# Optimization experiments

Measured on AMD Instinct MI355X. Metric: run time of the kernel, lower is better.

The kernel has to match this reference:

```python
import jax, jax.numpy as jnp
import numpy as np

N, E, G = 100000, 1600000, 256
D, H, O, DEPTH = 128, 128, 128, 3
BN_EPS = 1e-5
LN_EPS = 1e-5


def setup_inputs() -> dict:
    key = jax.random.key(0)
    ks = jax.random.split(key, 16)
    x = jax.random.normal(ks[0], (N, D), dtype=jnp.float32)
    edge_index = jax.random.randint(ks[1], (2, E), 0, N, dtype=jnp.int64)
    batch = jnp.sort(jax.random.randint(ks[2], (N,), 0, G, dtype=jnp.int64))
    s1 = 1.0 / np.sqrt(D)
    s2 = 1.0 / np.sqrt(H)
    return {
        "x": x,
        "edge_index": edge_index,
        "batch": batch,
        "W1s": jax.random.normal(ks[3], (DEPTH, D, H), dtype=jnp.float32) * s1,
        "b1s": jax.random.normal(ks[4], (DEPTH, H), dtype=jnp.float32) * 0.01,
        "bn_g": jnp.ones((DEPTH, H), dtype=jnp.float32),
        "bn_b": jnp.zeros((DEPTH, H), dtype=jnp.float32),
        "bn_m": jax.random.normal(ks[5], (DEPTH, H), dtype=jnp.float32) * 0.1,
        "bn_v": jax.random.uniform(ks[6], (DEPTH, H), dtype=jnp.float32, minval=0.5, maxval=1.5),
        "W2s": jax.random.normal(ks[7], (DEPTH, H, H), dtype=jnp.float32) * s2,
        "b2s": jax.random.normal(ks[8], (DEPTH, H), dtype=jnp.float32) * 0.01,
        "Wp": jax.random.normal(ks[9], (H, O), dtype=jnp.float32) * s2,
        "bp": jax.random.normal(ks[10], (O,), dtype=jnp.float32) * 0.01,
        "ln_g": jnp.ones((O,), dtype=jnp.float32),
        "ln_b": jnp.zeros((O,), dtype=jnp.float32),
    }


def reference(x, edge_index, batch, W1s, b1s, bn_g, bn_b, bn_m, bn_v, W2s, b2s, Wp, bp, ln_g, ln_b):
    src, dst = edge_index[0], edge_index[1]
    h = x
    for l in range(DEPTH):
        # GIN aggregation (eps=0): (1+eps)*h_i + sum_{j->i} h_j
        agg = jax.ops.segment_sum(h[src], dst, num_segments=N)  # [N, H]
        z = h + agg
        # MLP: Linear -> BatchNorm(eval) -> ReLU -> Linear
        z = z @ W1s[l] + b1s[l]
        z = (z - bn_m[l]) * jax.lax.rsqrt(bn_v[l] + BN_EPS) * bn_g[l] + bn_b[l]
        z = jax.nn.relu(z)
        z = z @ W2s[l] + b2s[l]
        # post-conv ReLU (dropout = identity in eval)
        h = jax.nn.relu(z)
    # global mean pool over graphs
    counts = jax.ops.segment_sum(jnp.ones((N,), h.dtype), batch, num_segments=G)
    hg = jax.ops.segment_sum(h, batch, num_segments=G) / jnp.maximum(counts, 1.0)[:, None]
    # proj: Linear + LayerNorm
    p = hg @ Wp + bp
    mu = jnp.mean(p, axis=-1, keepdims=True)
    var = jnp.var(p, axis=-1, keepdims=True)
    return (p - mu) * jax.lax.rsqrt(var + LN_EPS) * ln_g + ln_b
```

## Files before the change

kernel.cpp:

```cpp
#include <hip/hip_runtime.h>
#include <hip/hip_bf16.h>


#define GDEPTH 3
#define CAP 64

typedef __bf16 bf16x8 __attribute__((ext_vector_type(8)));
typedef float  f32x4  __attribute__((ext_vector_type(4)));
typedef __hip_bfloat16  bf16;
typedef __hip_bfloat162 bf162;

#define CSR_CH 2048
#define NSLICE 8
#define NSLICE_LOG 3

__global__ void k_setup(const float* __restrict__ W1s, const float* __restrict__ W2s,
                        const float* __restrict__ b1s, const float* __restrict__ bng,
                        const float* __restrict__ bnb, const float* __restrict__ bnm,
                        const float* __restrict__ bnv,
                        bf16* __restrict__ Wp1, bf16* __restrict__ Wp2,
                        float* __restrict__ sArr, float* __restrict__ tArr,
                        const float4* __restrict__ x4, bf162* __restrict__ h,
                        const int* __restrict__ batch, int* __restrict__ gp,
                        const int* __restrict__ ei, int* __restrict__ fill,
                        int* __restrict__ col,
                        int N, int E, int G, int BCONV, int BGB, int BCSR) {
    int bid = blockIdx.x;
    int tid = threadIdx.x;
    if (bid % 3 == 0 && bid / 3 < BCSR) {
        int sb = bid / 3;
        int s = sb & (NSLICE - 1);
        int chunk = sb >> NSLICE_LOG;
        int lo = (int)((long long)s * N / NSLICE);
        int hi = (int)((long long)(s + 1) * N / NSLICE);
        int baseq = chunk * (CSR_CH / 4);
        const int4* d4p = (const int4*)(ei + E);
        const int4* s4p = (const int4*)ei;
        #pragma unroll
        for (int i = 0; i < CSR_CH / 1024; ++i) {
            int q = baseq + i * 256 + tid;
            int e0 = q * 4;
            if (e0 + 3 < E) {
                int4 d4 = d4p[q];
                if ((d4.x >= lo && d4.x < hi) || (d4.y >= lo && d4.y < hi) ||
                    (d4.z >= lo && d4.z < hi) || (d4.w >= lo && d4.w < hi)) {
                    int4 s4 = s4p[q];
                    if (d4.x >= lo && d4.x < hi) { int p = atomicAdd(&fill[d4.x], 1); if (p < CAP) col[(size_t)d4.x * CAP + p] = s4.x; }
                    if (d4.y >= lo && d4.y < hi) { int p = atomicAdd(&fill[d4.y], 1); if (p < CAP) col[(size_t)d4.y * CAP + p] = s4.y; }
                    if (d4.z >= lo && d4.z < hi) { int p = atomicAdd(&fill[d4.z], 1); if (p < CAP) col[(size_t)d4.z * CAP + p] = s4.z; }
                    if (d4.w >= lo && d4.w < hi) { int p = atomicAdd(&fill[d4.w], 1); if (p < CAP) col[(size_t)d4.w * CAP + p] = s4.w; }
                }
            } else if (e0 < E) {
                for (int e = e0; e < E; ++e) {
                    int d = ei[E + e];
                    if (d >= lo && d < hi) {
                        int p = atomicAdd(&fill[d], 1);
                        if (p < CAP) col[(size_t)d * CAP + p] = ei[e];
                    }
                }
            }
        }
        return;
    }
    {
        int nsc = (bid + 2) / 3;
        if (nsc > BCSR) nsc = BCSR;
        bid -= nsc;
    }
    if (bid < 384) {
        int idx = bid * 256 + tid;
        int l   = idx / 32768;
        int rem = idx - l * 32768;
        int w   = rem >> 14;
        int p   = rem & 16383;
        int j = p & 7, n = (p >> 3) & 127, tq = p >> 10;
        int quad = tq & 3, kk = tq >> 2;
        int k = kk * 32 + quad * 8 + j;
        const float* W = w ? W2s : W1s;
        bf16* Wp = w ? Wp2 : Wp1;
        Wp[l * 16384 + p] = __float2bfloat16(W[l * 16384 + k * 128 + n]);
        if (idx < GDEPTH * 128) {
            int ll = idx >> 7, c = idx & 127;
            float inv = rsqrtf(bnv[ll * 128 + c] + 1e-5f);
            float s = inv * bng[ll * 128 + c];
            sArr[idx] = s;
            tArr[idx] = (b1s[ll * 128 + c] - bnm[ll * 128 + c]) * s + bnb[ll * 128 + c];
        }
        return;
    }
    bid -= 384;
    if (bid < BCONV) {
        int i = bid * 256 + tid;
        int n4 = N * 32;
        if (i < n4) {
            float4 v = x4[i];
            bf162 a, b;
            a.x = __float2bfloat16(v.x); a.y = __float2bfloat16(v.y);
            b.x = __float2bfloat16(v.z); b.y = __float2bfloat16(v.w);
            h[2 * i] = a; h[2 * i + 1] = b;
        }
        return;
    }
    bid -= BCONV;
    if (bid < BGB) {
        int i = bid * 256 + tid;
        if (i < N) {
            int b = batch[i];
            if (i == 0) {
                for (int g = 0; g <= b; ++g) gp[g] = 0;
            } else {
                int pb = batch[i - 1];
                if (pb != b) for (int g = pb + 1; g <= b; ++g) gp[g] = i;
            }
            if (i == N - 1) {
                for (int g = b + 1; g <= G; ++g) gp[g] = N;
            }
        }
        return;
    }
}

__global__ __launch_bounds__(256) void k_layer(const bf16* __restrict__ h,
                                               const int* __restrict__ deg,
                                               const int* __restrict__ col,
                                               const bf16* __restrict__ Bp1,
                                               const bf16* __restrict__ Bp2,
                                               const float* __restrict__ sv,
                                               const float* __restrict__ tv,
                                               const float* __restrict__ b2,
                                               bf16* __restrict__ Out, int M) {
    __shared__ __align__(16) bf16 As[32 * 136];
    const int tid = threadIdx.x;
    const int m0 = blockIdx.x * 32;
    const int grp = tid >> 4, c = tid & 15;
    const bf16x8* h8 = (const bf16x8*)h;

    #pragma unroll
    for (int it = 0; it < 2; ++it) {
        int row = grp * 2 + it;
        int node = m0 + row;
        float acc[8];
        if (node < M) {
            bf16x8 self = h8[(size_t)node * 16 + c];
            #pragma unroll
            for (int k = 0; k < 8; ++k) acc[k] = (float)self[k];
            int d = deg[node]; if (d > CAP) d = CAP;
            const int* cb = col + (size_t)node * CAP;
            int e = 0;
            for (; e + 3 < d; e += 4) {
                int j0 = cb[e], j1 = cb[e + 1], j2 = cb[e + 2], j3 = cb[e + 3];
                bf16x8 v0 = h8[(size_t)j0 * 16 + c];
                bf16x8 v1 = h8[(size_t)j1 * 16 + c];
                bf16x8 v2 = h8[(size_t)j2 * 16 + c];
                bf16x8 v3 = h8[(size_t)j3 * 16 + c];
                #pragma unroll
                for (int k = 0; k < 8; ++k)
                    acc[k] += ((float)v0[k] + (float)v1[k]) + ((float)v2[k] + (float)v3[k]);
            }
            for (; e < d; ++e) {
                bf16x8 v = h8[(size_t)cb[e] * 16 + c];
                #pragma unroll
                for (int k = 0; k < 8; ++k) acc[k] += (float)v[k];
            }
        } else {
            #pragma unroll
            for (int k = 0; k < 8; ++k) acc[k] = 0.f;
        }
        bf16x8 r;
        #pragma unroll
        for (int k = 0; k < 8; ++k) {
            __hip_bfloat16 t = __float2bfloat16(acc[k]);
            r[k] = *(__bf16*)&t;
        }
        *(bf16x8*)(As + row * 136 + c * 8) = r;
    }
    __syncthreads();

    const int lane = tid & 63;
    const int wid = tid >> 6;
    const int wm = wid & 1, wn = wid >> 1;
    const int l15 = lane & 15, quad = lane >> 4;

    f32x4 acc[4];
    #pragma unroll
    for (int j = 0; j < 4; ++j) acc[j] = (f32x4){0.f, 0.f, 0.f, 0.f};
    #pragma unroll
    for (int kk = 0; kk < 4; ++kk) {
        bf16x8 a, b[4];
        #pragma unroll
        for (int tn = 0; tn < 4; ++tn)
            b[tn] = *(const bf16x8*)(Bp1 + ((kk * 4 + quad) * 128 + wn * 64 + tn * 16 + l15) * 8);
        a = *(const bf16x8*)(As + (wm * 16 + l15) * 136 + kk * 32 + quad * 8);
        #pragma unroll
        for (int tn = 0; tn < 4; ++tn)
            acc[tn] = __builtin_amdgcn_mfma_f32_16x16x32_bf16(a, b[tn], acc[tn], 0, 0, 0);
    }
    __syncthreads();
    #pragma unroll
    for (int tn = 0; tn < 4; ++tn) {
        int gc = wn * 64 + tn * 16 + l15;
        float scale = sv[gc], shift = tv[gc];
        #pragma unroll
        for (int r = 0; r < 4; ++r) {
            float v = fmaxf(acc[tn][r] * scale + shift, 0.f);
            int row = wm * 16 + quad * 4 + r;
            __hip_bfloat16 t = __float2bfloat16(v);
            As[row * 136 + gc] = *(bf16*)&t;
        }
    }
    __syncthreads();
    #pragma unroll
    for (int j = 0; j < 4; ++j) acc[j] = (f32x4){0.f, 0.f, 0.f, 0.f};
    #pragma unroll
    for (int kk = 0; kk < 4; ++kk) {
        bf16x8 a, b[4];
        #pragma unroll
        for (int tn = 0; tn < 4; ++tn)
            b[tn] = *(const bf16x8*)(Bp2 + ((kk * 4 + quad) * 128 + wn * 64 + tn * 16 + l15) * 8);
        a = *(const bf16x8*)(As + (wm * 16 + l15) * 136 + kk * 32 + quad * 8);
        #pragma unroll
        for (int tn = 0; tn < 4; ++tn)
            acc[tn] = __builtin_amdgcn_mfma_f32_16x16x32_bf16(a, b[tn], acc[tn], 0, 0, 0);
    }
    #pragma unroll
    for (int tn = 0; tn < 4; ++tn) {
        int gc = wn * 64 + tn * 16 + l15;
        float shift = b2[gc];
        #pragma unroll
        for (int r = 0; r < 4; ++r) {
            int gr = m0 + wm * 16 + quad * 4 + r;
            if (gr < M) {
                float v = fmaxf(acc[tn][r] + shift, 0.f);
                Out[(size_t)gr * 128 + gc] = __float2bfloat16(v);
            }
        }
    }
}

#define PCH 128
__global__ void k_pool(const bf16* __restrict__ h, const int* __restrict__ batch,
                       float* __restrict__ hga, int N) {
    int base = blockIdx.x * PCH;
    if (base >= N) return;
    int t = threadIdx.x;
    int end = base + PCH; if (end > N) end = N;
    int gcur = batch[base];
    float acc = 0.f;
    for (int i = base; i < end; ++i) {
        int g = batch[i];
        if (g != gcur) {
            atomicAdd(&hga[gcur * 128 + t], acc);
            acc = 0.f; gcur = g;
        }
        acc += __bfloat162float(h[(size_t)i * 128 + t]);
    }
    atomicAdd(&hga[gcur * 128 + t], acc);
}

__global__ void k_proj_ln(const float* __restrict__ hga, const int* __restrict__ gp,
                          const float* __restrict__ Wp,
                          const float* __restrict__ bp, const float* __restrict__ lng,
                          const float* __restrict__ lnb, float* __restrict__ out) {
    __shared__ float row[128];
    __shared__ float red[128];
    int g = blockIdx.x, t = threadIdx.x;
    int cntn = gp[g + 1] - gp[g];
    float inv = 1.0f / (float)(cntn < 1 ? 1 : cntn);
    row[t] = hga[g * 128 + t] * inv;
    __syncthreads();
    float p = bp[t];
    #pragma unroll 8
    for (int k = 0; k < 128; ++k) p += row[k] * Wp[k * 128 + t];
    red[t] = p; __syncthreads();
    for (int o = 64; o > 0; o >>= 1) { if (t < o) red[t] += red[t + o]; __syncthreads(); }
    float mu = red[0] * (1.0f / 128.0f);
    __syncthreads();
    float d = p - mu;
    red[t] = d * d; __syncthreads();
    for (int o = 64; o > 0; o >>= 1) { if (t < o) red[t] += red[t + o]; __syncthreads(); }
    float var = red[0] * (1.0f / 128.0f);
    out[g * 128 + t] = d * rsqrtf(var + 1e-5f) * lng[t] + lnb[t];
}

extern "C" void kernel_launch(void* const* d_in, const int* in_sizes, int n_in,
                              void* d_out, int out_size, void* d_ws, size_t ws_size,
                              hipStream_t stream) {
    const float* x   = (const float*)d_in[0];
    const int*   ei  = (const int*)d_in[1];
    const int*   bat = (const int*)d_in[2];
    const float* W1s = (const float*)d_in[3];
    const float* b1s = (const float*)d_in[4];
    const float* bng = (const float*)d_in[5];
    const float* bnb = (const float*)d_in[6];
    const float* bnm = (const float*)d_in[7];
    const float* bnv = (const float*)d_in[8];
    const float* W2s = (const float*)d_in[9];
    const float* b2s = (const float*)d_in[10];
    const float* Wp  = (const float*)d_in[11];
    const float* bp  = (const float*)d_in[12];
    const float* lng = (const float*)d_in[13];
    const float* lnb = (const float*)d_in[14];
    const int E = in_sizes[1] / 2;
    const int N = in_sizes[2];
    const int G = out_size / 128;

    char* w = (char*)d_ws;
    size_t off = 0;
    auto alloc = [&](size_t b) { char* p = w + off; off += (b + 255) & ~(size_t)255; return p; };
    bf16* buf_a = (bf16*)alloc((size_t)N * 128 * 2);
    bf16* buf_b = (bf16*)alloc((size_t)N * 128 * 2);
    int* col   = (int*)alloc(((size_t)N * CAP + 256) * 4);
    int* fill  = (int*)alloc((size_t)N * 4);
    float* hga = (float*)alloc((size_t)G * 128 * 4);
    int* gp    = (int*)alloc(2048);
    bf16* Wp1  = (bf16*)alloc((size_t)GDEPTH * 16384 * 2);
    bf16* Wp2  = (bf16*)alloc((size_t)GDEPTH * 16384 * 2);
    float* sA  = (float*)alloc((size_t)GDEPTH * 128 * 4);
    float* tA  = (float*)alloc((size_t)GDEPTH * 128 * 4);

    size_t zlen = (size_t)((char*)hga + (size_t)G * 128 * 4 - (char*)fill);
    hipMemsetAsync(fill, 0, zlen, stream);

    const int BCONV = (N * 32 + 255) / 256;
    const int BGB   = (N + 255) / 256;
    const int BCSR  = ((E + CSR_CH - 1) / CSR_CH) * NSLICE;
    k_setup<<<384 + BCONV + BGB + BCSR, 256, 0, stream>>>(
        W1s, W2s, b1s, bng, bnb, bnm, bnv, Wp1, Wp2, sA, tA,
        (const float4*)x, (bf162*)buf_a, bat, gp, ei, fill, col, N, E, G, BCONV, BGB, BCSR);

    const bf16* hcur = buf_a;
    bf16* hnext = buf_b;
    for (int l = 0; l < GDEPTH; ++l) {
        k_layer<<<(N + 31) / 32, 256, 0, stream>>>(hcur, fill, col,
                                                   Wp1 + (size_t)l * 16384,
                                                   Wp2 + (size_t)l * 16384,
                                                   sA + l * 128, tA + l * 128,
                                                   b2s + l * 128, hnext, N);
        bf16* tmp = hnext; hnext = (bf16*)hcur; hcur = tmp;
    }
    k_pool<<<(N + PCH - 1) / PCH, 128, 0, stream>>>(hcur, bat, hga, N);
    k_proj_ln<<<G, 128, 0, stream>>>(hga, gp, Wp, bp, lng, lnb, (float*)d_out);
}
```

Before: 472.3 us.

## Fuse layers, pooling and projection into one persistent cooperative kernel

Replaces the three per-layer launches plus the pool and projection kernels with a single cooperative persistent kernel. Blocks loop over row tiles and use grid-wide syncs between layers and phases. The aim is to remove launch overhead and the tail gaps between kernels. The trade-offs are grid.sync costs, a grid capped by occupancy (up to 2048 blocks with a launch bound of 4 per SM), and a pooling phase that uses fewer parallel chunks per block.

```diff
diff --git a/kernel.cpp b/kernel.cpp
--- a/kernel.cpp
+++ b/kernel.cpp
@@ -1,9 +1,13 @@
 #include <hip/hip_runtime.h>
 #include <hip/hip_bf16.h>
+#include <hip/hip_cooperative_groups.h>
+
+namespace cg = cooperative_groups;
 
 
 #define GDEPTH 3
 #define CAP 64
+#define PCH 128
 
 typedef __bf16 bf16x8 __attribute__((ext_vector_type(8)));
 typedef float  f32x4  __attribute__((ext_vector_type(4)));
@@ -120,166 +124,192 @@
     }
 }
 
-__global__ __launch_bounds__(256) void k_layer(const bf16* __restrict__ h,
-                                               const int* __restrict__ deg,
-                                               const int* __restrict__ col,
-                                               const bf16* __restrict__ Bp1,
-                                               const bf16* __restrict__ Bp2,
-                                               const float* __restrict__ sv,
-                                               const float* __restrict__ tv,
-                                               const float* __restrict__ b2,
-                                               bf16* __restrict__ Out, int M) {
-    __shared__ __align__(16) bf16 As[32 * 136];
+__global__ __launch_bounds__(256, 4) void k_mega(
+        bf16* __restrict__ bufA, bf16* __restrict__ bufB,
+        const int* __restrict__ deg, const int* __restrict__ col,
+        const bf16* __restrict__ Wp1, const bf16* __restrict__ Wp2,
+        const float* __restrict__ sAr, const float* __restrict__ tAr,
+        const float* __restrict__ b2s,
+        const int* __restrict__ batch, const int* __restrict__ gp,
+        float* __restrict__ hga,
+        const float* __restrict__ Wpj, const float* __restrict__ bpj,
+        const float* __restrict__ lng, const float* __restrict__ lnb,
+        float* __restrict__ outp,
+        int N, int G, int NT, int NB) {
+    cg::grid_group gg = cg::this_grid();
+    __shared__ __align__(16) char smem[32 * 136 * 2];
+    bf16* As = (bf16*)smem;
     const int tid = threadIdx.x;
-    const int m0 = blockIdx.x * 32;
-    const int grp = tid >> 4, c = tid & 15;
-    const bf16x8* h8 = (const bf16x8*)h;
-
-    #pragma unroll
-    for (int it = 0; it < 2; ++it) {
-        int row = grp * 2 + it;
-        int node = m0 + row;
-        float acc[8];
-        if (node < M) {
-            bf16x8 self = h8[(size_t)node * 16 + c];
-            #pragma unroll
-            for (int k = 0; k < 8; ++k) acc[k] = (float)self[k];
-            int d = deg[node]; if (d > CAP) d = CAP;
-            const int* cb = col + (size_t)node * CAP;
-            int e = 0;
-            for (; e + 3 < d; e += 4) {
-                int j0 = cb[e], j1 = cb[e + 1], j2 = cb[e + 2], j3 = cb[e + 3];
-                bf16x8 v0 = h8[(size_t)j0 * 16 + c];
-                bf16x8 v1 = h8[(size_t)j1 * 16 + c];
-                bf16x8 v2 = h8[(size_t)j2 * 16 + c];
-                bf16x8 v3 = h8[(size_t)j3 * 16 + c];
-                #pragma unroll
-                for (int k = 0; k < 8; ++k)
-                    acc[k] += ((float)v0[k] + (float)v1[k]) + ((float)v2[k] + (float)v3[k]);
-            }
-            for (; e < d; ++e) {
-                bf16x8 v = h8[(size_t)cb[e] * 16 + c];
-                #pragma unroll
-                for (int k = 0; k < 8; ++k) acc[k] += (float)v[k];
-            }
-        } else {
-            #pragma unroll
-            for (int k = 0; k < 8; ++k) acc[k] = 0.f;
-        }
-        bf16x8 r;
-        #pragma unroll
-        for (int k = 0; k < 8; ++k) {
-            __hip_bfloat16 t = __float2bfloat16(acc[k]);
-            r[k] = *(__bf16*)&t;
-        }
-        *(bf16x8*)(As + row * 136 + c * 8) = r;
-    }
-    __syncthreads();
-
-    const int lane = tid & 63;
-    const int wid = tid >> 6;
-    const int wm = wid & 1, wn = wid >> 1;
-    const int l15 = lane & 15, quad = lane >> 4;
-
-    f32x4 acc[4];
-    #pragma unroll
-    for (int j = 0; j < 4; ++j) acc[j] = (f32x4){0.f, 0.f, 0.f, 0.f};
-    #pragma unroll
-    for (int kk = 0; kk < 4; ++kk) {
-        bf16x8 a, b[4];
-        #pragma unroll
-        for (int tn = 0; tn < 4; ++tn)
-            b[tn] = *(const bf16x8*)(Bp1 + ((kk * 4 + quad) * 128 + wn * 64 + tn * 16 + l15) * 8);
-        a = *(const bf16x8*)(As + (wm * 16 + l15) * 136 + kk * 32 + quad * 8);
-        #pragma unroll
-        for (int tn = 0; tn < 4; ++tn)
-            acc[tn] = __builtin_amdgcn_mfma_f32_16x16x32_bf16(a, b[tn], acc[tn], 0, 0, 0);
-    }
-    __syncthreads();
-    #pragma unroll
-    for (int tn = 0; tn < 4; ++tn) {
-        int gc = wn * 64 + tn * 16 + l15;
-        float scale = sv[gc], shift = tv[gc];
-        #pragma unroll
-        for (int r = 0; r < 4; ++r) {
-            float v = fmaxf(acc[tn][r] * scale + shift, 0.f);
-            int row = wm * 16 + quad * 4 + r;
-            __hip_bfloat16 t = __float2bfloat16(v);
-            As[row * 136 + gc] = *(bf16*)&t;
-        }
-    }
-    __syncthreads();
-    #pragma unroll
-    for (int j = 0; j < 4; ++j) acc[j] = (f32x4){0.f, 0.f, 0.f, 0.f};
-    #pragma unroll
-    for (int kk = 0; kk < 4; ++kk) {
-        bf16x8 a, b[4];
-        #pragma unroll
-        for (int tn = 0; tn < 4; ++tn)
-            b[tn] = *(const bf16x8*)(Bp2 + ((kk * 4 + quad) * 128 + wn * 64 + tn * 16 + l15) * 8);
-        a = *(const bf16x8*)(As + (wm * 16 + l15) * 136 + kk * 32 + quad * 8);
-        #pragma unroll
-        for (int tn = 0; tn < 4; ++tn)
-            acc[tn] = __builtin_amdgcn_mfma_f32_16x16x32_bf16(a, b[tn], acc[tn], 0, 0, 0);
-    }
-    #pragma unroll
-    for (int tn = 0; tn < 4; ++tn) {
-        int gc = wn * 64 + tn * 16 + l15;
-        float shift = b2[gc];
-        #pragma unroll
-        for (int r = 0; r < 4; ++r) {
-            int gr = m0 + wm * 16 + quad * 4 + r;
-            if (gr < M) {
-                float v = fmaxf(acc[tn][r] + shift, 0.f);
-                Out[(size_t)gr * 128 + gc] = __float2bfloat16(v);
-            }
-        }
-    }
-}
-
-#define PCH 128
-__global__ void k_pool(const bf16* __restrict__ h, const int* __restrict__ batch,
-                       float* __restrict__ hga, int N) {
-    int base = blockIdx.x * PCH;
-    if (base >= N) return;
-    int t = threadIdx.x;
-    int end = base + PCH; if (end > N) end = N;
-    int gcur = batch[base];
-    float acc = 0.f;
-    for (int i = base; i < end; ++i) {
-        int g = batch[i];
-        if (g != gcur) {
+
+    for (int l = 0; l < GDEPTH; ++l) {
+        const bf16* h = (l & 1) ? bufB : bufA;
+        bf16* Out = (l & 1) ? bufA : bufB;
+        const bf16* Bp1 = Wp1 + (size_t)l * 16384;
+        const bf16* Bp2 = Wp2 + (size_t)l * 16384;
+        const float* sv = sAr + l * 128;
+        const float* tv = tAr + l * 128;
+        const float* b2 = b2s + l * 128;
+        const bf16x8* h8 = (const bf16x8*)h;
+
+        for (int tile = blockIdx.x; tile < NT; tile += NB) {
+            const int m0 = tile * 32;
+            const int grp = tid >> 4, c = tid & 15;
+            #pragma unroll
+            for (int it = 0; it < 2; ++it) {
+                int row = grp * 2 + it;
+                int node = m0 + row;
+                float acc[8];
+                if (node < N) {
+                    bf16x8 self = h8[(size_t)node * 16 + c];
+                    #pragma unroll
+                    for (int k = 0; k < 8; ++k) acc[k] = (float)self[k];
+                    int d = deg[node]; if (d > CAP) d = CAP;
+                    const int* cb = col + (size_t)node * CAP;
+                    int e = 0;
+                    for (; e + 3 < d; e += 4) {
+                        int j0 = cb[e], j1 = cb[e + 1], j2 = cb[e + 2], j3 = cb[e + 3];
+                        bf16x8 v0 = h8[(size_t)j0 * 16 + c];
+                        bf16x8 v1 = h8[(size_t)j1 * 16 + c];
+                        bf16x8 v2 = h8[(size_t)j2 * 16 + c];
+                        bf16x8 v3 = h8[(size_t)j3 * 16 + c];
+                        #pragma unroll
+                        for (int k = 0; k < 8; ++k)
+                            acc[k] += ((float)v0[k] + (float)v1[k]) + ((float)v2[k] + (float)v3[k]);
+                    }
+                    for (; e < d; ++e) {
+                        bf16x8 v = h8[(size_t)cb[e] * 16 + c];
+                        #pragma unroll
+                        for (int k = 0; k < 8; ++k) acc[k] += (float)v[k];
+                    }
+                } else {
+                    #pragma unroll
+                    for (int k = 0; k < 8; ++k) acc[k] = 0.f;
+                }
+                bf16x8 r;
+                #pragma unroll
+                for (int k = 0; k < 8; ++k) {
+                    __hip_bfloat16 t = __float2bfloat16(acc[k]);
+                    r[k] = *(__bf16*)&t;
+                }
+                *(bf16x8*)(As + row * 136 + c * 8) = r;
+            }
+            __syncthreads();
+
+            const int lane = tid & 63;
+            const int wid = tid >> 6;
+            const int wm = wid & 1, wn = wid >> 1;
+            const int l15 = lane & 15, quad = lane >> 4;
+
+            f32x4 acc[4];
+            #pragma unroll
+            for (int j = 0; j < 4; ++j) acc[j] = (f32x4){0.f, 0.f, 0.f, 0.f};
+            #pragma unroll
+            for (int kk = 0; kk < 4; ++kk) {
+                bf16x8 a, b[4];
+                #pragma unroll
+                for (int tn = 0; tn < 4; ++tn)
+                    b[tn] = *(const bf16x8*)(Bp1 + ((kk * 4 + quad) * 128 + wn * 64 + tn * 16 + l15) * 8);
+                a = *(const bf16x8*)(As + (wm * 16 + l15) * 136 + kk * 32 + quad * 8);
+                #pragma unroll
+                for (int tn = 0; tn < 4; ++tn)
+                    acc[tn] = __builtin_amdgcn_mfma_f32_16x16x32_bf16(a, b[tn], acc[tn], 0, 0, 0);
+            }
+            __syncthreads();
+            #pragma unroll
+            for (int tn = 0; tn < 4; ++tn) {
+                int gc = wn * 64 + tn * 16 + l15;
+                float scale = sv[gc], shift = tv[gc];
+                #pragma unroll
+                for (int r = 0; r < 4; ++r) {
+                    float v = fmaxf(acc[tn][r] * scale + shift, 0.f);
+                    int row = wm * 16 + quad * 4 + r;
+                    __hip_bfloat16 t = __float2bfloat16(v);
+                    As[row * 136 + gc] = *(bf16*)&t;
+                }
+            }
+            __syncthreads();
+            #pragma unroll
+            for (int j = 0; j < 4; ++j) acc[j] = (f32x4){0.f, 0.f, 0.f, 0.f};
+            #pragma unroll
+            for (int kk = 0; kk < 4; ++kk) {
+                bf16x8 a, b[4];
+                #pragma unroll
+                for (int tn = 0; tn < 4; ++tn)
+                    b[tn] = *(const bf16x8*)(Bp2 + ((kk * 4 + quad) * 128 + wn * 64 + tn * 16 + l15) * 8);
+                a = *(const bf16x8*)(As + (wm * 16 + l15) * 136 + kk * 32 + quad * 8);
+                #pragma unroll
+                for (int tn = 0; tn < 4; ++tn)
+                    acc[tn] = __builtin_amdgcn_mfma_f32_16x16x32_bf16(a, b[tn], acc[tn], 0, 0, 0);
+            }
+            #pragma unroll
+            for (int tn = 0; tn < 4; ++tn) {
+                int gc = wn * 64 + tn * 16 + l15;
+                float shift = b2[gc];
+                #pragma unroll
+                for (int r = 0; r < 4; ++r) {
+                    int gr = m0 + wm * 16 + quad * 4 + r;
+                    if (gr < N) {
+                        float v = fmaxf(acc[tn][r] + shift, 0.f);
+                        Out[(size_t)gr * 128 + gc] = __float2bfloat16(v);
+                    }
+                }
+            }
+            __syncthreads();
+        }
+        gg.sync();
+    }
+
+    const bf16* hf = (GDEPTH & 1) ? bufB : bufA;
+    {
+        int sub = tid >> 7, t = tid & 127;
+        for (int ch = blockIdx.x * 2 + sub; ch * PCH < N; ch += NB * 2) {
+            int base = ch * PCH;
+            int end = base + PCH; if (end > N) end = N;
+            int gcur = batch[base];
+            float acc = 0.f;
+            for (int i = base; i < end; ++i) {
+                int g = batch[i];
+                if (g != gcur) {
+                    atomicAdd(&hga[gcur * 128 + t], acc);
+                    acc = 0.f; gcur = g;
+                }
+                acc += __bfloat162float(hf[(size_t)i * 128 + t]);
+            }
             atomicAdd(&hga[gcur * 128 + t], acc);
-            acc = 0.f; gcur = g;
-        }
-        acc += __bfloat162float(h[(size_t)i * 128 + t]);
-    }
-    atomicAdd(&hga[gcur * 128 + t], acc);
-}
-
-__global__ void k_proj_ln(const float* __restrict__ hga, const int* __restrict__ gp,
-                          const float* __restrict__ Wp,
-                          const float* __restrict__ bp, const float* __restrict__ lng,
-                          const float* __restrict__ lnb, float* __restrict__ out) {
-    __shared__ float row[128];
-    __shared__ float red[128];
-    int g = blockIdx.x, t = threadIdx.x;
-    int cntn = gp[g + 1] - gp[g];
-    float inv = 1.0f / (float)(cntn < 1 ? 1 : cntn);
-    row[t] = hga[g * 128 + t] * inv;
-    __syncthreads();
-    float p = bp[t];
-    #pragma unroll 8
-    for (int k = 0; k < 128; ++k) p += row[k] * Wp[k * 128 + t];
-    red[t] = p; __syncthreads();
-    for (int o = 64; o > 0; o >>= 1) { if (t < o) red[t] += red[t + o]; __syncthreads(); }
-    float mu = red[0] * (1.0f / 128.0f);
-    __syncthreads();
-    float d = p - mu;
-    red[t] = d * d; __syncthreads();
-    for (int o = 64; o > 0; o >>= 1) { if (t < o) red[t] += red[t + o]; __syncthreads(); }
-    float var = red[0] * (1.0f / 128.0f);
-    out[g * 128 + t] = d * rsqrtf(var + 1e-5f) * lng[t] + lnb[t];
+        }
+    }
+    gg.sync();
+
+    {
+        float* prow = (float*)smem;
+        float* pred = (float*)(smem + 512);
+        for (int g = blockIdx.x; g < G; g += NB) {
+            float p = 0.f;
+            if (tid < 128) {
+                int cntn = gp[g + 1] - gp[g];
+                float inv = 1.0f / (float)(cntn < 1 ? 1 : cntn);
+                prow[tid] = hga[g * 128 + tid] * inv;
+            }
+            __syncthreads();
+            if (tid < 128) {
+                p = bpj[tid];
+                #pragma unroll 8
+                for (int k = 0; k < 128; ++k) p += prow[k] * Wpj[k * 128 + tid];
+                pred[tid] = p;
+            }
+            __syncthreads();
+            for (int o = 64; o > 0; o >>= 1) { if (tid < o) pred[tid] += pred[tid + o]; __syncthreads(); }
+            float mu = pred[0] * (1.0f / 128.0f);
+            __syncthreads();
+            if (tid < 128) pred[tid] = (p - mu) * (p - mu);
+            __syncthreads();
+            for (int o = 64; o > 0; o >>= 1) { if (tid < o) pred[tid] += pred[tid + o]; __syncthreads(); }
+            float var = pred[0] * (1.0f / 128.0f);
+            if (tid < 128)
+                outp[g * 128 + tid] = (p - mu) * rsqrtf(var + 1e-5f) * lng[tid] + lnb[tid];
+            __syncthreads();
+        }
+    }
 }
 
 extern "C" void kernel_launch(void* const* d_in, const int* in_sizes, int n_in,
@@ -328,16 +358,23 @@
         W1s, W2s, b1s, bng, bnb, bnm, bnv, Wp1, Wp2, sA, tA,
         (const float4*)x, (bf162*)buf_a, bat, gp, ei, fill, col, N, E, G, BCONV, BGB, BCSR);
 
-    const bf16* hcur = buf_a;
-    bf16* hnext = buf_b;
-    for (int l = 0; l < GDEPTH; ++l) {
-        k_layer<<<(N + 31) / 32, 256, 0, stream>>>(hcur, fill, col,
-                                                   Wp1 + (size_t)l * 16384,
-                                                   Wp2 + (size_t)l * 16384,
-                                                   sA + l * 128, tA + l * 128,
-                                                   b2s + l * 128, hnext, N);
-        bf16* tmp = hnext; hnext = (bf16*)hcur; hcur = tmp;
-    }
-    k_pool<<<(N + PCH - 1) / PCH, 128, 0, stream>>>(hcur, bat, hga, N);
-    k_proj_ln<<<G, 128, 0, stream>>>(hga, gp, Wp, bp, lng, lnb, (float*)d_out);
+    static int s_nb = 0;
+    if (s_nb == 0) {
+        int mb = 0;
+        if (hipOccupancyMaxActiveBlocksPerMultiprocessor(&mb, k_mega, 256, 0) != hipSuccess || mb < 1)
+            mb = 4;
+        s_nb = mb * 256;
+        if (s_nb > 2048) s_nb = 2048;
+    }
+    int NT = (N + 31) / 32;
+    int NB = s_nb;
+    float* outp = (float*)d_out;
+    void* args[] = {
+        (void*)&buf_a, (void*)&buf_b, (void*)&fill, (void*)&col,
+        (void*)&Wp1, (void*)&Wp2, (void*)&sA, (void*)&tA,
+        (void*)&b2s, (void*)&bat, (void*)&gp, (void*)&hga,
+        (void*)&Wp, (void*)&bp, (void*)&lng, (void*)&lnb, (void*)&outp,
+        (void*)&N, (void*)&G, (void*)&NT, (void*)&NB
+    };
+    hipLaunchCooperativeKernel((void*)k_mega, dim3(NB), dim3(256), args, 0, stream);
 }
```

Result: slower. 915.5 us (+93.8%).
